# Optimization experiments

Measured on AMD Instinct MI355X. Metric: run time of the kernel, lower is better.

The kernel has to match this reference:

```python
import jax, jax.numpy as jnp
import numpy as np

N_NODES = 50000
N_EDGES = 1600000
E_DIM = 128
N_LAYERS = 3
N_GRAPHS = 32


def setup_inputs() -> dict:
    key = jax.random.key(0)
    ks = jax.random.split(key, 12)
    x = jax.random.normal(ks[0], (N_NODES,), dtype=jnp.float32)
    edge_index = jax.random.randint(ks[1], (2, N_EDGES), 0, N_NODES, dtype=jnp.int32)
    batch = jnp.sort(jax.random.randint(ks[2], (N_NODES,), 0, N_GRAPHS, dtype=jnp.int32))
    s_in = 1.0  # fan_in = 1 for the first linear
    s_e = 1.0 / np.sqrt(E_DIM)
    lin_w = jax.random.normal(ks[3], (1, E_DIM), jnp.float32) * s_in
    lin_b = jax.random.normal(ks[4], (E_DIM,), jnp.float32) * 0.01
    gcn_w = jax.random.normal(ks[5], (N_LAYERS, E_DIM, E_DIM), jnp.float32) * s_e
    gcn_b = jax.random.normal(ks[6], (N_LAYERS, E_DIM), jnp.float32) * 0.01
    r1_w = jax.random.normal(ks[7], (E_DIM, E_DIM), jnp.float32) * s_e
    r1_b = jax.random.normal(ks[8], (E_DIM,), jnp.float32) * 0.01
    r2_w = jax.random.normal(ks[9], (E_DIM, 1), jnp.float32) * s_e
    r2_b = jax.random.normal(ks[10], (1,), jnp.float32) * 0.01
    return {"x": x, "edge_index": edge_index, "batch": batch,
            "lin_w": lin_w, "lin_b": lin_b, "gcn_w": gcn_w, "gcn_b": gcn_b,
            "r1_w": r1_w, "r1_b": r1_b, "r2_w": r2_w, "r2_b": r2_b}


def reference(x, edge_index, batch, lin_w, lin_b, gcn_w, gcn_b, r1_w, r1_b, r2_w, r2_b):
    # input embedding: x.view(-1, 1) @ W + b -> [N, E]
    h = x.reshape(-1, 1) @ lin_w + lin_b

    # GCN normalization (add self-loops, symmetric deg^-1/2 norm) — structure is
    # identical across layers, so compute once.
    loops = jnp.arange(N_NODES, dtype=edge_index.dtype)
    src = jnp.concatenate([edge_index[0], loops])
    dst = jnp.concatenate([edge_index[1], loops])
    deg = jax.ops.segment_sum(jnp.ones(src.shape[0], h.dtype), dst, num_segments=N_NODES)
    dinv = jnp.where(deg > 0, jax.lax.rsqrt(deg), 0.0)
    norm = (dinv[src] * dinv[dst])[:, None]  # [E+N, 1]

    # NOTE: original calls x.relu() without assignment -> no activation (faithful).
    for l in range(N_LAYERS):
        h = h @ gcn_w[l]                                        # [N, E]
        h = jax.ops.segment_sum(h[src] * norm, dst, num_segments=N_NODES) + gcn_b[l]

    # global_add_pool over graphs
    pooled = jax.ops.segment_sum(h, batch, num_segments=N_GRAPHS)  # [G, E]
    hr = jnp.tanh(pooled @ r1_w + r1_b)
    return hr @ r2_w + r2_b  # [G, 1]
```

## Files before the change

kernel.cpp:

```cpp
#include <hip/hip_runtime.h>
#include <hip/hip_bf16.h>
#include <math.h>

#define NGRAPH 32
#define CAP 10240
#define EPT 24
#define EPB (256 * EPT)

__global__ void k_part(const int* __restrict__ src, const int* __restrict__ dst,
                       int* __restrict__ gcursor, unsigned int* __restrict__ packed, int E) {
    __shared__ unsigned int ldsbuf[EPB];
    __shared__ int hist[256], lofs[256], lcur[256], base[256];
    int tid = threadIdx.x;
    int e0 = blockIdx.x * EPB;
    hist[tid] = 0;
    __syncthreads();
    int d[EPT], s[EPT];
#pragma unroll
    for (int c = 0; c < EPT / 4; c++) {
        int e = e0 + c * 1024 + (tid << 2);
        if (e + 3 < E) {
            int4 dv = *(const int4*)&dst[e];
            int4 sv = *(const int4*)&src[e];
            d[4*c+0] = dv.x; d[4*c+1] = dv.y; d[4*c+2] = dv.z; d[4*c+3] = dv.w;
            s[4*c+0] = sv.x; s[4*c+1] = sv.y; s[4*c+2] = sv.z; s[4*c+3] = sv.w;
            atomicAdd(&hist[dv.x >> 8], 1);
            atomicAdd(&hist[dv.y >> 8], 1);
            atomicAdd(&hist[dv.z >> 8], 1);
            atomicAdd(&hist[dv.w >> 8], 1);
        } else {
#pragma unroll
            for (int k = 0; k < 4; k++) {
                int ee = e + k;
                if (ee < E) {
                    d[4*c+k] = dst[ee]; s[4*c+k] = src[ee];
                    atomicAdd(&hist[d[4*c+k] >> 8], 1);
                } else {
                    d[4*c+k] = -1;
                }
            }
        }
    }
    __syncthreads();
    int v = hist[tid];
    lofs[tid] = v;
    __syncthreads();
    for (int off = 1; off < 256; off <<= 1) {
        int t = (tid >= off) ? lofs[tid - off] : 0;
        __syncthreads();
        lofs[tid] += t;
        __syncthreads();
    }
    int total = lofs[255];
    int excl = lofs[tid] - v;
    lofs[tid] = excl;
    lcur[tid] = excl;
    if (v > 0) base[tid] = tid * CAP + atomicAdd(&gcursor[tid], v);
    __syncthreads();
#pragma unroll
    for (int c = 0; c < EPT; c++) {
        int dd = d[c];
        if (dd >= 0) {
            int bk = dd >> 8;
            int slot = atomicAdd(&lcur[bk], 1);
            ldsbuf[slot] = ((unsigned int)bk << 24) | ((unsigned int)s[c] << 8)
                         | (unsigned int)(dd & 255);
        }
    }
    __syncthreads();
    for (int i = tid; i < total; i += 256) {
        unsigned int w = ldsbuf[i];
        int bk = w >> 24;
        packed[base[bk] + (i - lofs[bk])] = w & 0xFFFFFFu;
    }
}

__global__ void k_bucket(const unsigned int* __restrict__ packed, const int* __restrict__ gcursor,
                         const float* __restrict__ x, const int* __restrict__ batch,
                         int* __restrict__ offs, int* __restrict__ deg,
                         float* __restrict__ dinv, float2* __restrict__ q0,
                         unsigned short* __restrict__ csr, float* __restrict__ S, int N) {
    __shared__ int cnt[256], lofs[256], lcur[256];
    __shared__ float cs[NGRAPH];
    int tid = threadIdx.x;
    int b = blockIdx.x;
    int start = b * CAP;
    int end = start + gcursor[b];
    cnt[tid] = 0;
    if (tid < NGRAPH) cs[tid] = 0.f;
    __syncthreads();
    for (int e = start + tid; e < end; e += 256)
        atomicAdd(&cnt[packed[e] & 255], 1);
    __syncthreads();
    int v = cnt[tid];
    int vp = (v + 1) & ~1;
    lofs[tid] = vp;
    __syncthreads();
    for (int off = 1; off < 256; off <<= 1) {
        int t = (tid >= off) ? lofs[tid - off] : 0;
        __syncthreads();
        lofs[tid] += t;
        __syncthreads();
    }
    int excl = lofs[tid] - vp;
    lcur[tid] = excl;
    int node = b * 256 + tid;
    if (node < N) {
        deg[node] = v;
        offs[node] = start + excl;
        float dv = rsqrtf((float)(v + 1));
        dinv[node] = dv;
        q0[node] = make_float2(x[node] * dv, dv);
        atomicAdd(&cs[batch[node]], 1.f);
    }
    __syncthreads();
    for (int e = start + tid; e < end; e += 256) {
        unsigned int p = packed[e];
        int pos = start + atomicAdd(&lcur[p & 255], 1);
        csr[pos] = (unsigned short)(p >> 8);
    }
    if (tid < NGRAPH && cs[tid] != 0.f) atomicAdd(&S[tid], cs[tid]);
}

template <int WRITE_Q>
__global__ void k_hop(const float2* __restrict__ qin, float2* __restrict__ outv,
                      const unsigned short* __restrict__ csr,
                      const int* __restrict__ offs, const int* __restrict__ deg,
                      const float* __restrict__ dinv, int N) {
    int tid = threadIdx.x;
    int lane = tid & 15;
    int node = blockIdx.x * 16 + (tid >> 4);
    if (node >= N) return;
    int e = offs[node], ne = deg[node];
    float sx = 0.0f, su = 0.0f;
    for (int j = 2 * lane; j < ne; j += 32) {
        ushort2 c = *(const ushort2*)&csr[e + j];
        float2 a = qin[c.x];
        sx += a.x; su += a.y;
        if (j + 1 < ne) {
            float2 b = qin[c.y];
            sx += b.x; su += b.y;
        }
    }
#pragma unroll
    for (int m = 8; m > 0; m >>= 1) {
        sx += __shfl_xor(sx, m);
        su += __shfl_xor(su, m);
    }
    if (lane == 0) {
        float2 qs = qin[node];
        float dv = dinv[node];
        float px = dv * (sx + qs.x), pu = dv * (su + qs.y);
        if (WRITE_Q) outv[node] = make_float2(px * dv, pu * dv);
        else         outv[node] = make_float2(px, pu);
    }
}

__global__ void k_mlp(const float* __restrict__ S,
                      const float2* __restrict__ q1, const float2* __restrict__ q2,
                      const float2* __restrict__ p3, const float* __restrict__ dinv,
                      const float* __restrict__ lin_w, const float* __restrict__ lin_b,
                      const float* __restrict__ gcn_w, const float* __restrict__ gcn_b,
                      const float* __restrict__ r1_w, const float* __restrict__ r1_b,
                      const float* __restrict__ r2_w, const float* __restrict__ r2_b,
                      float* __restrict__ out, int N) {
    __shared__ float va[128], vb[128], vc[128], vd[128], pl[128], red[128];
    __shared__ float cnts[NGRAPH];
    __shared__ float r4[4 * 128];
    int j = threadIdx.x;
    int g = blockIdx.x;
    if (j < NGRAPH) cnts[j] = S[j];
    __syncthreads();
    int r0 = 0;
    for (int i = 0; i < g; i++) r0 += (int)cnts[i];
    int cnt = (int)cnts[g];
    int r1 = r0 + cnt;
    float su1 = 0.f, su2 = 0.f, su3 = 0.f, sv3 = 0.f;
    for (int n = r0 + j; n < r1; n += 128) {
        float inv = 1.0f / dinv[n];
        su1 += q1[n].y * inv;
        su2 += q2[n].y * inv;
        float2 p = p3[n];
        su3 += p.y; sv3 += p.x;
    }
    r4[j] = su1; r4[128 + j] = su2; r4[256 + j] = su3; r4[384 + j] = sv3;
    __syncthreads();
    for (int sft = 64; sft > 0; sft >>= 1) {
        if (j < sft) {
            r4[j] += r4[j + sft];
            r4[128 + j] += r4[128 + j + sft];
            r4[256 + j] += r4[256 + j + sft];
            r4[384 + j] += r4[384 + j + sft];
        }
        __syncthreads();
    }
    su1 = r4[0]; su2 = r4[128]; su3 = r4[256]; sv3 = r4[384];
    va[j] = lin_w[j];
    vb[j] = lin_b[j];
    vc[j] = gcn_b[j];
    vd[j] = gcn_b[128 + j];
    __syncthreads();
    for (int l = 0; l < 3; l++) {
        const float* W = gcn_w + l * 128 * 128;
        float na = 0.f, nb = 0.f, nc = 0.f, nd = 0.f;
        for (int k = 0; k < 128; k++) {
            float w = W[k * 128 + j];
            na += va[k] * w;
            nb += vb[k] * w;
            nc += vc[k] * w;
            nd += vd[k] * w;
        }
        __syncthreads();
        va[j] = na; vb[j] = nb;
        if (l >= 1) vc[j] = nc;
        if (l >= 2) vd[j] = nd;
        __syncthreads();
    }
    const float* b3 = gcn_b + 2 * 128;
    pl[j] = sv3 * va[j] + su3 * vb[j] + su2 * vc[j] + su1 * vd[j] + (float)cnt * b3[j];
    __syncthreads();
    float acc = r1_b[j];
#pragma unroll 4
    for (int k = 0; k < 128; k++) acc += pl[k] * r1_w[k * 128 + j];
    red[j] = tanhf(acc) * r2_w[j];
    __syncthreads();
    for (int sft = 64; sft > 0; sft >>= 1) {
        if (j < sft) red[j] += red[j + sft];
        __syncthreads();
    }
    if (j == 0) out[g] = red[0] + r2_b[0];
}

extern "C" void kernel_launch(void* const* d_in, const int* in_sizes, int n_in,
                              void* d_out, int out_size, void* d_ws, size_t ws_size,
                              hipStream_t stream) {
    const float* x     = (const float*)d_in[0];
    const int*   eidx  = (const int*)d_in[1];
    const int*   batch = (const int*)d_in[2];
    const float* lin_w = (const float*)d_in[3];
    const float* lin_b = (const float*)d_in[4];
    const float* gcn_w = (const float*)d_in[5];
    const float* gcn_b = (const float*)d_in[6];
    const float* r1_w  = (const float*)d_in[7];
    const float* r1_b  = (const float*)d_in[8];
    const float* r2_w  = (const float*)d_in[9];
    const float* r2_b  = (const float*)d_in[10];

    const int N = in_sizes[0];
    const int E = in_sizes[1] / 2;
    const int* src = eidx;
    const int* dst = eidx + E;
    const int NB = (N + 255) / 256;

    char* w = (char*)d_ws;
    float2* q0      = (float2*)w; w += (size_t)N * 8;
    float2* q1      = (float2*)w; w += (size_t)N * 8;
    float2* q2      = (float2*)w; w += (size_t)N * 8;
    float2* p3      = (float2*)w; w += (size_t)N * 8;
    unsigned int* packed = (unsigned int*)w; w += (size_t)256 * CAP * 4;
    int*    offs    = (int*)w;    w += (size_t)N * 4;
    int*    deg     = (int*)w;    w += (size_t)N * 4;
    float*  dinv    = (float*)w;  w += (size_t)N * 4;
    int*    gcursor = (int*)w;    w += 256 * 4;
    float*  S       = (float*)w;  w += 64 * 4;
    unsigned short* csr = (unsigned short*)w; w += (size_t)256 * CAP * 2 + 256;

    hipMemsetAsync(gcursor, 0, 256 * 4 + 64 * 4, stream);

    k_part<<<(E + EPB - 1) / EPB, 256, 0, stream>>>(src, dst, gcursor, packed, E);
    k_bucket<<<NB, 256, 0, stream>>>(packed, gcursor, x, batch, offs, deg, dinv, q0, csr, S, N);

    int hop_blocks = (N + 15) / 16;
    k_hop<1><<<hop_blocks, 256, 0, stream>>>(q0, q1, csr, offs, deg, dinv, N);
    k_hop<1><<<hop_blocks, 256, 0, stream>>>(q1, q2, csr, offs, deg, dinv, N);
    k_hop<0><<<hop_blocks, 256, 0, stream>>>(q2, p3, csr, offs, deg, dinv, N);

    k_mlp<<<NGRAPH, 128, 0, stream>>>(S, q1, q2, p3, dinv, lin_w, lin_b, gcn_w, gcn_b,
                                      r1_w, r1_b, r2_w, r2_b, (float*)d_out, N);
}
```

Baseline: 177.0 us.

## Split weight-chain matvecs into single wide kernel and parallelize MLP tail

The per-graph MLP kernel used to recompute the three 128x128 weight-chain matvecs serially in every one of the 32 blocks. That work now runs once, in a separate 1024-thread kernel that stages each weight matrix in LDS and splits the k-dimension across 8 thread groups. The MLP kernel grows to 256 threads, stages r1_w in LDS, reduces with wavefront shuffles, and splits the r1 matvec in two halves. This trades redundant, serially dependent work for one extra kernel launch and larger LDS use.

```diff
diff --git a/kernel.cpp b/kernel.cpp
--- a/kernel.cpp
+++ b/kernel.cpp
@@ -156,79 +156,131 @@
     }
 }
 
-__global__ void k_mlp(const float* __restrict__ S,
-                      const float2* __restrict__ q1, const float2* __restrict__ q2,
-                      const float2* __restrict__ p3, const float* __restrict__ dinv,
-                      const float* __restrict__ lin_w, const float* __restrict__ lin_b,
-                      const float* __restrict__ gcn_w, const float* __restrict__ gcn_b,
-                      const float* __restrict__ r1_w, const float* __restrict__ r1_b,
-                      const float* __restrict__ r2_w, const float* __restrict__ r2_b,
-                      float* __restrict__ out, int N) {
-    __shared__ float va[128], vb[128], vc[128], vd[128], pl[128], red[128];
+__global__ __launch_bounds__(1024) void k_chain(
+        const float* __restrict__ lin_w, const float* __restrict__ lin_b,
+        const float* __restrict__ gcn_w, const float* __restrict__ gcn_b,
+        float* __restrict__ chainv) {
+    __shared__ float W[128 * 128];
+    __shared__ float v4[4 * 128];
+    __shared__ float part[4 * 128 * 8];
+    int tid = threadIdx.x;
+    int j = tid & 127;
+    int ch = tid >> 7;
+    if (tid < 128) {
+        v4[tid]       = lin_w[tid];
+        v4[128 + tid] = lin_b[tid];
+        v4[256 + tid] = gcn_b[tid];
+        v4[384 + tid] = gcn_b[128 + tid];
+    }
+    for (int l = 0; l < 3; l++) {
+        __syncthreads();
+        const float4* Wg = (const float4*)(gcn_w + l * 128 * 128);
+        float4* Ws = (float4*)W;
+#pragma unroll
+        for (int i = 0; i < 4; i++) Ws[tid + i * 1024] = Wg[tid + i * 1024];
+        __syncthreads();
+        float na = 0.f, nb = 0.f, nc = 0.f, nd = 0.f;
+#pragma unroll
+        for (int kk = 0; kk < 16; kk++) {
+            int k = ch * 16 + kk;
+            float w = W[k * 128 + j];
+            na += v4[k] * w;
+            nb += v4[128 + k] * w;
+            nc += v4[256 + k] * w;
+            nd += v4[384 + k] * w;
+        }
+        part[(0 * 128 + j) * 8 + ch] = na;
+        part[(1 * 128 + j) * 8 + ch] = nb;
+        part[(2 * 128 + j) * 8 + ch] = nc;
+        part[(3 * 128 + j) * 8 + ch] = nd;
+        __syncthreads();
+        if (tid < 512) {
+            int vec = tid >> 7, jj = tid & 127;
+            float s = 0.f;
+#pragma unroll
+            for (int c = 0; c < 8; c++) s += part[(vec * 128 + jj) * 8 + c];
+            if (vec < 2 || (vec == 2 && l >= 1) || (vec == 3 && l >= 2))
+                v4[vec * 128 + jj] = s;
+        }
+    }
+    __syncthreads();
+    if (tid < 512) chainv[tid] = v4[tid];
+}
+
+__global__ __launch_bounds__(256) void k_mlp(
+        const float* __restrict__ S, const float* __restrict__ chainv,
+        const float2* __restrict__ q1, const float2* __restrict__ q2,
+        const float2* __restrict__ p3, const float* __restrict__ dinv,
+        const float* __restrict__ gcn_b,
+        const float* __restrict__ r1_w, const float* __restrict__ r1_b,
+        const float* __restrict__ r2_w, const float* __restrict__ r2_b,
+        float* __restrict__ out, int N) {
+    __shared__ float rw[128 * 128];
+    __shared__ float pl[128], red[128];
     __shared__ float cnts[NGRAPH];
     __shared__ float r4[4 * 128];
-    int j = threadIdx.x;
+    int tid = threadIdx.x;
     int g = blockIdx.x;
-    if (j < NGRAPH) cnts[j] = S[j];
+    {
+        const float4* Rg = (const float4*)r1_w;
+        float4* Rs = (float4*)rw;
+#pragma unroll
+        for (int i = 0; i < 16; i++) Rs[tid + i * 256] = Rg[tid + i * 256];
+    }
+    if (tid < NGRAPH) cnts[tid] = S[tid];
     __syncthreads();
     int r0 = 0;
     for (int i = 0; i < g; i++) r0 += (int)cnts[i];
     int cnt = (int)cnts[g];
     int r1 = r0 + cnt;
     float su1 = 0.f, su2 = 0.f, su3 = 0.f, sv3 = 0.f;
-    for (int n = r0 + j; n < r1; n += 128) {
+    for (int n = r0 + tid; n < r1; n += 256) {
         float inv = 1.0f / dinv[n];
         su1 += q1[n].y * inv;
         su2 += q2[n].y * inv;
         float2 p = p3[n];
         su3 += p.y; sv3 += p.x;
     }
-    r4[j] = su1; r4[128 + j] = su2; r4[256 + j] = su3; r4[384 + j] = sv3;
+#pragma unroll
+    for (int m = 32; m > 0; m >>= 1) {
+        su1 += __shfl_xor(su1, m);
+        su2 += __shfl_xor(su2, m);
+        su3 += __shfl_xor(su3, m);
+        sv3 += __shfl_xor(sv3, m);
+    }
+    int wv = tid >> 6;
+    if ((tid & 63) == 0) {
+        r4[wv] = su1; r4[4 + wv] = su2; r4[8 + wv] = su3; r4[12 + wv] = sv3;
+    }
+    __syncthreads();
+    su1 = r4[0] + r4[1] + r4[2] + r4[3];
+    su2 = r4[4] + r4[5] + r4[6] + r4[7];
+    su3 = r4[8] + r4[9] + r4[10] + r4[11];
+    sv3 = r4[12] + r4[13] + r4[14] + r4[15];
+    const float* b3 = gcn_b + 2 * 128;
+    if (tid < 128)
+        pl[tid] = sv3 * chainv[tid] + su3 * chainv[128 + tid] + su2 * chainv[256 + tid]
+                + su1 * chainv[384 + tid] + (float)cnt * b3[tid];
+    __syncthreads();
+    int j = tid & 127, half = tid >> 7;
+    float acc = 0.f;
+#pragma unroll
+    for (int kk = 0; kk < 64; kk++) {
+        int k = half * 64 + kk;
+        acc += pl[k] * rw[k * 128 + j];
+    }
+    r4[half * 128 + j] = acc;
+    __syncthreads();
+    if (tid < 128) {
+        float a = r4[tid] + r4[128 + tid] + r1_b[tid];
+        red[tid] = tanhf(a) * r2_w[tid];
+    }
     __syncthreads();
     for (int sft = 64; sft > 0; sft >>= 1) {
-        if (j < sft) {
-            r4[j] += r4[j + sft];
-            r4[128 + j] += r4[128 + j + sft];
-            r4[256 + j] += r4[256 + j + sft];
-            r4[384 + j] += r4[384 + j + sft];
-        }
-        __syncthreads();
-    }
-    su1 = r4[0]; su2 = r4[128]; su3 = r4[256]; sv3 = r4[384];
-    va[j] = lin_w[j];
-    vb[j] = lin_b[j];
-    vc[j] = gcn_b[j];
-    vd[j] = gcn_b[128 + j];
-    __syncthreads();
-    for (int l = 0; l < 3; l++) {
-        const float* W = gcn_w + l * 128 * 128;
-        float na = 0.f, nb = 0.f, nc = 0.f, nd = 0.f;
-        for (int k = 0; k < 128; k++) {
-            float w = W[k * 128 + j];
-            na += va[k] * w;
-            nb += vb[k] * w;
-            nc += vc[k] * w;
-            nd += vd[k] * w;
-        }
-        __syncthreads();
-        va[j] = na; vb[j] = nb;
-        if (l >= 1) vc[j] = nc;
-        if (l >= 2) vd[j] = nd;
-        __syncthreads();
-    }
-    const float* b3 = gcn_b + 2 * 128;
-    pl[j] = sv3 * va[j] + su3 * vb[j] + su2 * vc[j] + su1 * vd[j] + (float)cnt * b3[j];
-    __syncthreads();
-    float acc = r1_b[j];
-#pragma unroll 4
-    for (int k = 0; k < 128; k++) acc += pl[k] * r1_w[k * 128 + j];
-    red[j] = tanhf(acc) * r2_w[j];
-    __syncthreads();
-    for (int sft = 64; sft > 0; sft >>= 1) {
-        if (j < sft) red[j] += red[j + sft];
-        __syncthreads();
-    }
-    if (j == 0) out[g] = red[0] + r2_b[0];
+        if (tid < sft) red[tid] += red[tid + sft];
+        __syncthreads();
+    }
+    if (tid == 0) out[g] = red[0] + r2_b[0];
 }
 
 extern "C" void kernel_launch(void* const* d_in, const int* in_sizes, int n_in,
@@ -263,6 +315,7 @@
     float*  dinv    = (float*)w;  w += (size_t)N * 4;
     int*    gcursor = (int*)w;    w += 256 * 4;
     float*  S       = (float*)w;  w += 64 * 4;
+    float*  chainv  = (float*)w;  w += 512 * 4;
     unsigned short* csr = (unsigned short*)w; w += (size_t)256 * CAP * 2 + 256;
 
     hipMemsetAsync(gcursor, 0, 256 * 4 + 64 * 4, stream);
@@ -275,6 +328,7 @@
     k_hop<1><<<hop_blocks, 256, 0, stream>>>(q1, q2, csr, offs, deg, dinv, N);
     k_hop<0><<<hop_blocks, 256, 0, stream>>>(q2, p3, csr, offs, deg, dinv, N);
 
-    k_mlp<<<NGRAPH, 128, 0, stream>>>(S, q1, q2, p3, dinv, lin_w, lin_b, gcn_w, gcn_b,
+    k_chain<<<1, 1024, 0, stream>>>(lin_w, lin_b, gcn_w, gcn_b, chainv);
+    k_mlp<<<NGRAPH, 256, 0, stream>>>(S, chainv, q1, q2, p3, dinv, gcn_b,
                                       r1_w, r1_b, r2_w, r2_b, (float*)d_out, N);
 }
```

Measured after the change: 165.7 us. 6.4% less time.
